# Kernel tuning notes

Measured on AMD Instinct MI355X. Metric: run time of the kernel, lower is better.

Reference implementation:

```python
import jax, jax.numpy as jnp
import numpy as np

# Module hyperparameters (init_kwargs)
THRESHOLD_ABS = 0.2
THRESHOLD_REL = 0.05   # set to None to disable the relative-threshold branch
MIN_DISTANCE = 3


def setup_inputs() -> dict:
    key = jax.random.key(0)
    # belief maps in [0, 1), NCHW
    belive_map = jax.random.uniform(key, (32, 4, 512, 512), dtype=jnp.float32)
    return {"belive_map": belive_map}


def reference(belive_map):
    """Peak detection on belief maps (dense, jit-friendly form).

    Faithful to BeliveMapsNMS.forward: the torch module additionally compacts
    the mask into (coords, labels, scores) lists via nonzero/gather, which has
    data-dependent shapes; here we return the equivalent dense outputs:
      mask        [B,C,H,W] bool   - peak locations (nonzero of this == torch ind)
      scores_abs  [B,C,H,W] f32    - belief value at peaks, 0 elsewhere
      scores_rel  [B,C,H,W] f32    - scores_abs / per-(b,c) max
    """
    k = 2 * MIN_DISTANCE + 1          # 7
    pad = k // 2                       # 3 -> 'same' max pool, stride 1

    # F.max_pool2d(kernel=k, stride=1, padding=k//2)
    x_max = jax.lax.reduce_window(
        belive_map, -jnp.inf, jax.lax.max,
        window_dimensions=(1, 1, k, k),
        window_strides=(1, 1, 1, 1),
        padding=[(0, 0), (0, 0), (pad, pad), (pad, pad)],
    )

    # per-(batch, channel) global max: hh.max(dim=2) on the flattened map
    vmax = jnp.max(belive_map, axis=(2, 3), keepdims=True)  # [B,C,1,1]

    mask = (x_max == belive_map) & (belive_map > THRESHOLD_ABS)
    if THRESHOLD_REL is not None:
        mask = mask & (belive_map > THRESHOLD_REL * vmax)

    scores_abs = jnp.where(mask, belive_map, jnp.float32(0.0))
    scores_rel = scores_abs / vmax
    return mask, scores_abs, scores_rel
```

## Files before the change

### kernel.cpp

```cpp
#include <hip/hip_runtime.h>
#include <math.h>


#define H 512
#define W 512
#define PLANE_ELEMS (H * W)
#define TH 16
#define LROWS (TH + 6)
#define NEG_INF (-INFINITY)

typedef float v4f __attribute__((ext_vector_type(4)));

__device__ __forceinline__ float4 vmax4(float4 a, float4 b) {
    return make_float4(fmaxf(a.x, b.x), fmaxf(a.y, b.y), fmaxf(a.z, b.z), fmaxf(a.w, b.w));
}

__device__ __forceinline__ void nt_store4(float* p, float a, float b, float c, float d) {
    v4f v = {a, b, c, d};
    __builtin_nontemporal_store(v, (v4f*)p);
}

__global__ __launch_bounds__(256) void vmax_kernel(const float* __restrict__ in,
                                                   unsigned int* __restrict__ vmax_bits) {
    const int q = blockIdx.x;
    const int plane = blockIdx.y;
    const float4* p = (const float4*)(in + (size_t)plane * PLANE_ELEMS + q * (PLANE_ELEMS / 4));
    float m = 0.0f;
    const int nvec = PLANE_ELEMS / 4 / 4;
    for (int i = threadIdx.x; i < nvec; i += 256) {
        float4 v = p[i];
        m = fmaxf(m, fmaxf(fmaxf(v.x, v.y), fmaxf(v.z, v.w)));
    }
    #pragma unroll
    for (int o = 32; o > 0; o >>= 1) m = fmaxf(m, __shfl_down(m, o, 64));
    __shared__ float s[4];
    if ((threadIdx.x & 63) == 0) s[threadIdx.x >> 6] = m;
    __syncthreads();
    if (threadIdx.x == 0) {
        m = fmaxf(fmaxf(s[0], s[1]), fmaxf(s[2], s[3]));
        atomicMax(&vmax_bits[plane], __float_as_uint(m));
    }
}

__global__ __launch_bounds__(256) void nms_kernel(const float* __restrict__ in,
                                                  const unsigned int* __restrict__ vmax_bits,
                                                  float* __restrict__ out, int N) {
    const int plane = blockIdx.y;
    const int ty0 = blockIdx.x * TH;
    const float* pin = in + (size_t)plane * PLANE_ELEMS;

    __shared__ __align__(16) float sRow[LROWS * W];

    const int wid = threadIdx.x >> 6;
    const int lane = threadIdx.x & 63;
    const int c8 = lane << 3;

    for (int r = wid; r < LROWS; r += 4) {
        const int gy = ty0 + r - 3;
        float4 v0, v1;
        if (gy >= 0 && gy < H) {
            const float4* row = (const float4*)(pin + (size_t)gy * W);
            v0 = row[lane * 2];
            v1 = row[lane * 2 + 1];
        } else {
            v0 = v1 = make_float4(NEG_INF, NEG_INF, NEG_INF, NEG_INF);
        }
        float l0 = __shfl_up(v1.y, 1, 64), l1 = __shfl_up(v1.z, 1, 64), l2 = __shfl_up(v1.w, 1, 64);
        float r0 = __shfl_down(v0.x, 1, 64), r1 = __shfl_down(v0.y, 1, 64), r2 = __shfl_down(v0.z, 1, 64);
        if (lane == 0) { l0 = NEG_INF; l1 = NEG_INF; l2 = NEG_INF; }
        if (lane == 63) { r0 = NEG_INF; r1 = NEG_INF; r2 = NEG_INF; }
        float a[14] = {l0, l1, l2, v0.x, v0.y, v0.z, v0.w, v1.x, v1.y, v1.z, v1.w, r0, r1, r2};
        float A[7];
        A[6] = a[6];
        #pragma unroll
        for (int j = 5; j >= 0; --j) A[j] = fmaxf(a[j], A[j + 1]);
        float rm[8];
        rm[0] = A[0];
        float B = a[7];
        rm[1] = fmaxf(A[1], B);
        #pragma unroll
        for (int j = 2; j <= 6; ++j) { B = fmaxf(B, a[6 + j]); rm[j] = fmaxf(A[j], B); }
        B = fmaxf(B, a[13]);
        rm[7] = B;
        float4* dst = (float4*)&sRow[r * W + c8];
        dst[0] = make_float4(rm[0], rm[1], rm[2], rm[3]);
        dst[1] = make_float4(rm[4], rm[5], rm[6], rm[7]);
    }
    __syncthreads();

    const float vmax = __uint_as_float(vmax_bits[plane]);
    const float rel_thr = 0.05f * vmax;
    const float inv_vmax = 1.0f / vmax;

    float* __restrict__ omask = out;
    float* __restrict__ oabs = out + (size_t)N;
    float* __restrict__ orel = out + 2 * (size_t)N;

    const int strip = threadIdx.x >> 7;
    const int cg = threadIdx.x & 127;
    const int c = cg << 2;
    const int y0 = strip << 3;

    float4 Lr[7], Aq[7];
    #pragma unroll
    for (int k = 0; k < 7; ++k) Lr[k] = *(const float4*)&sRow[(y0 + k) * W + c];
    Aq[6] = Lr[6];
    #pragma unroll
    for (int j = 5; j >= 0; --j) Aq[j] = vmax4(Lr[j], Aq[j + 1]);

    const int gy_base = ty0 + y0;
    float4 Bq;
    #pragma unroll
    for (int i = 0; i < 8; ++i) {
        float4 m;
        if (i == 0) {
            m = Aq[0];
        } else {
            float4 row = *(const float4*)&sRow[(y0 + 6 + i) * W + c];
            Bq = (i == 1) ? row : vmax4(Bq, row);
            m = (i == 7) ? Bq : vmax4(Aq[i], Bq);
        }
        const int gy = gy_base + i;
        const float4 ctr = *(const float4*)(pin + (size_t)gy * W + c);
        const bool p0 = (m.x == ctr.x) & (ctr.x > 0.2f) & (ctr.x > rel_thr);
        const bool p1 = (m.y == ctr.y) & (ctr.y > 0.2f) & (ctr.y > rel_thr);
        const bool p2 = (m.z == ctr.z) & (ctr.z > 0.2f) & (ctr.z > rel_thr);
        const bool p3 = (m.w == ctr.w) & (ctr.w > 0.2f) & (ctr.w > rel_thr);
        const float a0 = p0 ? ctr.x : 0.0f, a1 = p1 ? ctr.y : 0.0f;
        const float a2 = p2 ? ctr.z : 0.0f, a3 = p3 ? ctr.w : 0.0f;
        const size_t o = (size_t)plane * PLANE_ELEMS + (size_t)gy * W + c;
        nt_store4(omask + o, p0 ? 1.0f : 0.0f, p1 ? 1.0f : 0.0f,
                             p2 ? 1.0f : 0.0f, p3 ? 1.0f : 0.0f);
        nt_store4(oabs + o, a0, a1, a2, a3);
        nt_store4(orel + o, a0 * inv_vmax, a1 * inv_vmax, a2 * inv_vmax, a3 * inv_vmax);
    }
}

extern "C" void kernel_launch(void* const* d_in, const int* in_sizes, int n_in,
                              void* d_out, int out_size, void* d_ws, size_t ws_size,
                              hipStream_t stream) {
    const float* in = (const float*)d_in[0];
    float* out = (float*)d_out;
    const int N = in_sizes[0];
    const int planes = N / PLANE_ELEMS;

    unsigned int* vmax_bits = (unsigned int*)d_ws;
    (void)hipMemsetAsync(vmax_bits, 0, planes * sizeof(unsigned int), stream);

    vmax_kernel<<<dim3(4, planes), 256, 0, stream>>>(in, vmax_bits);
    nms_kernel<<<dim3(H / TH, planes), 256, 0, stream>>>(in, vmax_bits, out, N);
}
```

Baseline: 491.7 us.

## Batch halo row loads, prefetch center rows before barrier, swizzle block order

```diff
diff --git a/kernel.cpp b/kernel.cpp
--- a/kernel.cpp
+++ b/kernel.cpp
@@ -45,8 +45,11 @@
 __global__ __launch_bounds__(256) void nms_kernel(const float* __restrict__ in,
                                                   const unsigned int* __restrict__ vmax_bits,
                                                   float* __restrict__ out, int N) {
-    const int plane = blockIdx.y;
-    const int ty0 = blockIdx.x * TH;
+    const int hwid = blockIdx.x + (blockIdx.y << 5);
+    const int wg = ((hwid & 7) << 9) + (hwid >> 3);
+    const int plane = wg >> 5;
+    const int ty0 = (wg & 31) * TH;
+
     const float* pin = in + (size_t)plane * PLANE_ELEMS;
 
     __shared__ __align__(16) float sRow[LROWS * W];
@@ -55,51 +58,71 @@
     const int lane = threadIdx.x & 63;
     const int c8 = lane << 3;
 
-    for (int r = wid; r < LROWS; r += 4) {
-        const int gy = ty0 + r - 3;
-        float4 v0, v1;
-        if (gy >= 0 && gy < H) {
-            const float4* row = (const float4*)(pin + (size_t)gy * W);
-            v0 = row[lane * 2];
-            v1 = row[lane * 2 + 1];
-        } else {
-            v0 = v1 = make_float4(NEG_INF, NEG_INF, NEG_INF, NEG_INF);
+    float4 va[6], vb[6];
+    #pragma unroll
+    for (int k = 0; k < 6; ++k) {
+        const int r = wid + (k << 2);
+        if (r < LROWS) {
+            const int gy = ty0 + r - 3;
+            if (gy >= 0 && gy < H) {
+                const float4* row = (const float4*)(pin + (size_t)gy * W);
+                va[k] = row[lane * 2];
+                vb[k] = row[lane * 2 + 1];
+            } else {
+                va[k] = vb[k] = make_float4(NEG_INF, NEG_INF, NEG_INF, NEG_INF);
+            }
         }
-        float l0 = __shfl_up(v1.y, 1, 64), l1 = __shfl_up(v1.z, 1, 64), l2 = __shfl_up(v1.w, 1, 64);
-        float r0 = __shfl_down(v0.x, 1, 64), r1 = __shfl_down(v0.y, 1, 64), r2 = __shfl_down(v0.z, 1, 64);
-        if (lane == 0) { l0 = NEG_INF; l1 = NEG_INF; l2 = NEG_INF; }
-        if (lane == 63) { r0 = NEG_INF; r1 = NEG_INF; r2 = NEG_INF; }
-        float a[14] = {l0, l1, l2, v0.x, v0.y, v0.z, v0.w, v1.x, v1.y, v1.z, v1.w, r0, r1, r2};
-        float A[7];
-        A[6] = a[6];
-        #pragma unroll
-        for (int j = 5; j >= 0; --j) A[j] = fmaxf(a[j], A[j + 1]);
-        float rm[8];
-        rm[0] = A[0];
-        float B = a[7];
-        rm[1] = fmaxf(A[1], B);
-        #pragma unroll
-        for (int j = 2; j <= 6; ++j) { B = fmaxf(B, a[6 + j]); rm[j] = fmaxf(A[j], B); }
-        B = fmaxf(B, a[13]);
-        rm[7] = B;
-        float4* dst = (float4*)&sRow[r * W + c8];
-        dst[0] = make_float4(rm[0], rm[1], rm[2], rm[3]);
-        dst[1] = make_float4(rm[4], rm[5], rm[6], rm[7]);
     }
-    __syncthreads();
+
+    #pragma unroll
+    for (int k = 0; k < 6; ++k) {
+        const int r = wid + (k << 2);
+        if (r < LROWS) {
+            float4 v0 = va[k], v1 = vb[k];
+            float l0 = __shfl_up(v1.y, 1, 64), l1 = __shfl_up(v1.z, 1, 64), l2 = __shfl_up(v1.w, 1, 64);
+            float r0 = __shfl_down(v0.x, 1, 64), r1 = __shfl_down(v0.y, 1, 64), r2 = __shfl_down(v0.z, 1, 64);
+            if (lane == 0) { l0 = NEG_INF; l1 = NEG_INF; l2 = NEG_INF; }
+            if (lane == 63) { r0 = NEG_INF; r1 = NEG_INF; r2 = NEG_INF; }
+            float a[14] = {l0, l1, l2, v0.x, v0.y, v0.z, v0.w, v1.x, v1.y, v1.z, v1.w, r0, r1, r2};
+            float A[7];
+            A[6] = a[6];
+            #pragma unroll
+            for (int j = 5; j >= 0; --j) A[j] = fmaxf(a[j], A[j + 1]);
+            float rm[8];
+            rm[0] = A[0];
+            float B = a[7];
+            rm[1] = fmaxf(A[1], B);
+            #pragma unroll
+            for (int j = 2; j <= 6; ++j) { B = fmaxf(B, a[6 + j]); rm[j] = fmaxf(A[j], B); }
+            B = fmaxf(B, a[13]);
+            rm[7] = B;
+            float4* dst = (float4*)&sRow[r * W + c8];
+            dst[0] = make_float4(rm[0], rm[1], rm[2], rm[3]);
+            dst[1] = make_float4(rm[4], rm[5], rm[6], rm[7]);
+        }
+    }
+
+    const int strip = threadIdx.x >> 7;
+    const int cg = threadIdx.x & 127;
+    const int c = cg << 2;
+    const int y0 = strip << 3;
+    const int gy_base = ty0 + y0;
+
+    float4 ctr[8];
+    #pragma unroll
+    for (int i = 0; i < 8; ++i) {
+        ctr[i] = *(const float4*)(pin + (size_t)(gy_base + i) * W + c);
+    }
 
     const float vmax = __uint_as_float(vmax_bits[plane]);
     const float rel_thr = 0.05f * vmax;
     const float inv_vmax = 1.0f / vmax;
 
+    __syncthreads();
+
     float* __restrict__ omask = out;
     float* __restrict__ oabs = out + (size_t)N;
     float* __restrict__ orel = out + 2 * (size_t)N;
-
-    const int strip = threadIdx.x >> 7;
-    const int cg = threadIdx.x & 127;
-    const int c = cg << 2;
-    const int y0 = strip << 3;
 
     float4 Lr[7], Aq[7];
     #pragma unroll
@@ -108,7 +131,6 @@
     #pragma unroll
     for (int j = 5; j >= 0; --j) Aq[j] = vmax4(Lr[j], Aq[j + 1]);
 
-    const int gy_base = ty0 + y0;
     float4 Bq;
     #pragma unroll
     for (int i = 0; i < 8; ++i) {
@@ -121,13 +143,13 @@
             m = (i == 7) ? Bq : vmax4(Aq[i], Bq);
         }
         const int gy = gy_base + i;
-        const float4 ctr = *(const float4*)(pin + (size_t)gy * W + c);
-        const bool p0 = (m.x == ctr.x) & (ctr.x > 0.2f) & (ctr.x > rel_thr);
-        const bool p1 = (m.y == ctr.y) & (ctr.y > 0.2f) & (ctr.y > rel_thr);
-        const bool p2 = (m.z == ctr.z) & (ctr.z > 0.2f) & (ctr.z > rel_thr);
-        const bool p3 = (m.w == ctr.w) & (ctr.w > 0.2f) & (ctr.w > rel_thr);
-        const float a0 = p0 ? ctr.x : 0.0f, a1 = p1 ? ctr.y : 0.0f;
-        const float a2 = p2 ? ctr.z : 0.0f, a3 = p3 ? ctr.w : 0.0f;
+        const float4 cc = ctr[i];
+        const bool p0 = (m.x == cc.x) & (cc.x > 0.2f) & (cc.x > rel_thr);
+        const bool p1 = (m.y == cc.y) & (cc.y > 0.2f) & (cc.y > rel_thr);
+        const bool p2 = (m.z == cc.z) & (cc.z > 0.2f) & (cc.z > rel_thr);
+        const bool p3 = (m.w == cc.w) & (cc.w > 0.2f) & (cc.w > rel_thr);
+        const float a0 = p0 ? cc.x : 0.0f, a1 = p1 ? cc.y : 0.0f;
+        const float a2 = p2 ? cc.z : 0.0f, a3 = p3 ? cc.w : 0.0f;
         const size_t o = (size_t)plane * PLANE_ELEMS + (size_t)gy * W + c;
         nt_store4(omask + o, p0 ? 1.0f : 0.0f, p1 ? 1.0f : 0.0f,
                              p2 ? 1.0f : 0.0f, p3 ? 1.0f : 0.0f);
```

New measurement: 486.6 us. About the same (-1.0%).
